# Performance work log

Hardware: AMD Instinct MI355X
Metric: run time of the kernel (lower is better)

The kernel has to match this reference:

```python
import jax, jax.numpy as jnp
import numpy as np

N, E, D_IN, D_H = 20000, 320000, 512, 512
ALPHA = 0.1
LAMBDA = 1.0

def setup_inputs() -> dict:
    key = jax.random.key(0)
    ks = jax.random.split(key, 12)
    feat = jax.random.normal(ks[0], (N, D_IN), dtype=jnp.float32)
    src = jax.random.randint(ks[1], (E,), 0, N, dtype=jnp.int32)
    dst = jax.random.randint(ks[2], (E,), 0, N, dtype=jnp.int32)
    s = 0.05
    fc_w = jax.random.normal(ks[3], (D_H, D_IN), dtype=jnp.float32) * s  # torch Linear: [out,in]
    fc_b = jax.random.normal(ks[4], (D_H,), dtype=jnp.float32) * s
    w1_1 = jax.random.normal(ks[5], (D_H, D_H), dtype=jnp.float32) * s
    w2_1 = jax.random.normal(ks[6], (D_H, D_H), dtype=jnp.float32) * s
    b_1 = jax.random.normal(ks[7], (D_H,), dtype=jnp.float32) * s
    w1_2 = jax.random.normal(ks[8], (D_H, D_H), dtype=jnp.float32) * s
    w2_2 = jax.random.normal(ks[9], (D_H, D_H), dtype=jnp.float32) * s
    b_2 = jax.random.normal(ks[10], (D_H,), dtype=jnp.float32) * s
    return {"feat": feat, "src": src, "dst": dst, "fc_w": fc_w, "fc_b": fc_b,
            "w1_1": w1_1, "w2_1": w2_1, "b_1": b_1,
            "w1_2": w1_2, "w2_2": w2_2, "b_2": b_2}


def _gcn2_layer(h, h0, src, dst, norm, w1, w2, b, layer):
    # DGL GCN2Conv (project_initial_features=False)
    beta = float(np.log(LAMBDA / layer + 1.0))
    x = h * norm                      # [N, D]
    agg = jax.ops.segment_sum(x[src], dst, num_segments=h.shape[0])  # SpMM: sum over in-neighbors
    agg = agg * norm
    f = agg * (1.0 - ALPHA)
    f0 = h0 * ALPHA
    rst = ((1.0 - beta) * f + beta * (f @ w1)
           + (1.0 - beta) * f0 + beta * (f0 @ w2) + b)
    return jax.nn.relu(rst)


def reference(feat, src, dst, fc_w, fc_b, w1_1, w2_1, b_1, w1_2, w2_2, b_2):
    n = feat.shape[0]
    h = feat @ fc_w.T + fc_b          # initial projection
    # symmetric norm from in-degrees (clamped at 1), as in DGL
    deg = jax.ops.segment_sum(jnp.ones_like(dst, dtype=h.dtype), dst, num_segments=n)
    norm = jnp.clip(deg, 1.0, None) ** -0.5
    norm = norm[:, None]
    res = _gcn2_layer(h, h, src, dst, norm, w1_1, w2_1, b_1, layer=1)
    out = _gcn2_layer(res, h, src, dst, norm, w1_2, w2_2, b_2, layer=2)
    return out
```

## Files before the change

kernel.cpp:

```cpp
#include <hip/hip_runtime.h>
#include <hip/hip_bf16.h>
#include <stdint.h>
#include <stddef.h>

typedef __bf16 bf16_t;
typedef __bf16 bf16x4 __attribute__((ext_vector_type(4)));
typedef __bf16 bf16x8 __attribute__((ext_vector_type(8)));
typedef float floatx4 __attribute__((ext_vector_type(4)));

#define NN 20000
#define EE 320000
#define DD 512
#define CAP 96
#define BETA1 0.6931471805599453f
#define BETA2 0.40546510810816444f

__device__ __forceinline__ void gload16(const bf16_t* g, bf16_t* l) {
  __builtin_amdgcn_global_load_lds((const __attribute__((address_space(1))) uint32_t*)g,
                                   (__attribute__((address_space(3))) uint32_t*)l, 16, 0, 0);
}

__global__ __launch_bounds__(256) void bucket_kernel(
    const int* __restrict__ src, const int* __restrict__ dst,
    int* __restrict__ cnt, int* __restrict__ esrc, int E) {
  int e = blockIdx.x * 256 + threadIdx.x;
  if (e < E) {
    int d = dst[e];
    int pos = atomicAdd(&cnt[d], 1);
    if (pos < CAP) esrc[d * CAP + pos] = src[e];
  }
}

#define PREP_BLOCKS 8106
__global__ __launch_bounds__(256) void prep_kernel(
    const float* __restrict__ feat, const float* __restrict__ fc_w,
    const float* __restrict__ w1_1, const float* __restrict__ w2_1,
    const float* __restrict__ w1_2, const float* __restrict__ w2_2,
    bf16_t* __restrict__ featb, bf16_t* __restrict__ bw0,
    bf16_t* __restrict__ bt1, bf16_t* __restrict__ bt2,
    int* __restrict__ cnt, int* __restrict__ esrc) {
  __shared__ bf16_t tile[32][33];
  int b = blockIdx.x, t = threadIdx.x;
  if (b < 5128) {
    const float* in = (b < 5000) ? feat : fc_w;
    bf16_t* out = (b < 5000) ? featb : bw0;
    size_t c = (size_t)(b < 5000 ? b : b - 5000) * 256 + t;
    const float* s = in + c * 8;
    float4 v0 = *(const float4*)s, v1 = *(const float4*)(s + 4);
    bf16x8 o = {(bf16_t)v0.x, (bf16_t)v0.y, (bf16_t)v0.z, (bf16_t)v0.w,
                (bf16_t)v1.x, (bf16_t)v1.y, (bf16_t)v1.z, (bf16_t)v1.w};
    *(bf16x8*)(out + c * 8) = o;
  } else if (b < 6152) {
    int base = (b < 5640) ? 5128 : 5640;
    const float* Wa = (b < 5640) ? w1_1 : w1_2;
    const float* Wb = (b < 5640) ? w2_1 : w2_2;
    bf16_t* bt = (b < 5640) ? bt1 : bt2;
    int bb = b - base;
    int n0 = (bb & 15) * 32;
    int k0 = (bb >> 4) * 32;
    int tx = t & 31, ty = t >> 5;
    const float* W = (k0 < 512) ? Wa : Wb;
    float sc = (k0 < 512) ? 1.0f : 0.1f;
    int kk = k0 & 511;
#pragma unroll
    for (int i = 0; i < 32; i += 8)
      tile[ty + i][tx] = (bf16_t)(sc * W[(size_t)(kk + ty + i) * 512 + n0 + tx]);
    __syncthreads();
#pragma unroll
    for (int i = 0; i < 32; i += 8)
      bt[(size_t)(n0 + ty + i) * 1024 + k0 + tx] = tile[tx][ty + i];
  } else if (b < 6231) {
    int i = (b - 6152) * 256 + t;
    if (i < NN) cnt[i] = 0;
  } else {
    int i = (b - 6231) * 256 + t;
    ((int4*)esrc)[i] = make_int4(0, 0, 0, 0);
  }
}

__global__ __launch_bounds__(256) void aggregate_kernel(
    const bf16_t* __restrict__ hs, const int* __restrict__ cnt,
    const int* __restrict__ esrc, bf16_t* __restrict__ Acat) {
  __shared__ bf16_t ring[4][3][4][512];
  const int w = threadIdx.x >> 6;
  const int lane = threadIdx.x & 63;
  const int node = blockIdx.x * 4 + w;
  const int* eb = esrc + (size_t)node * CAP;
  int ncnt = cnt[node];
  int n_e = ncnt < CAP ? ncnt : CAP;
  float nd = 0.9f * rsqrtf(fmaxf((float)ncnt, 1.0f));
  int nchunks = (n_e + 3) >> 2;

  float acc[8] = {};
  bf16_t* rb0 = &ring[w][0][0][lane * 8];
  bf16_t* rb1 = &ring[w][1][0][lane * 8];
  bf16_t* rb2 = &ring[w][2][0][lane * 8];

  asm volatile("s_waitcnt vmcnt(0)" ::: "memory");
  __builtin_amdgcn_sched_barrier(0);
  int4 i0 = *(const int4*)(eb);
  asm volatile("s_waitcnt vmcnt(0)" ::: "memory");
  __builtin_amdgcn_sched_barrier(0);
  int4 i1 = *(const int4*)(eb + 4);
  asm volatile("s_waitcnt vmcnt(0)" ::: "memory");
  __builtin_amdgcn_sched_barrier(0);
  gload16(hs + (size_t)i0.x * DD + lane * 8, rb0);
  gload16(hs + (size_t)i0.y * DD + lane * 8, rb0 + 512);
  gload16(hs + (size_t)i0.z * DD + lane * 8, rb0 + 1024);
  gload16(hs + (size_t)i0.w * DD + lane * 8, rb0 + 1536);
  int4 inext = *(const int4*)(eb + 8);
  gload16(hs + (size_t)i1.x * DD + lane * 8, rb1);
  gload16(hs + (size_t)i1.y * DD + lane * 8, rb1 + 512);
  gload16(hs + (size_t)i1.z * DD + lane * 8, rb1 + 1024);
  gload16(hs + (size_t)i1.w * DD + lane * 8, rb1 + 1536);

  for (int c = 0; c < nchunks; ++c) {
    asm volatile("s_waitcnt vmcnt(4)" ::: "memory");
    __builtin_amdgcn_sched_barrier(0);
    int4 iuse = inext;
    int off = (c + 3) * 4; off = off > CAP - 4 ? CAP - 4 : off;
    inext = *(const int4*)(eb + off);
    bf16_t* rbn = (c % 3 == 0) ? rb2 : (c % 3 == 1) ? rb0 : rb1;
    gload16(hs + (size_t)iuse.x * DD + lane * 8, rbn);
    gload16(hs + (size_t)iuse.y * DD + lane * 8, rbn + 512);
    gload16(hs + (size_t)iuse.z * DD + lane * 8, rbn + 1024);
    gload16(hs + (size_t)iuse.w * DD + lane * 8, rbn + 1536);
    bf16_t* rb = (c % 3 == 0) ? rb0 : (c % 3 == 1) ? rb1 : rb2;
    bf16x8 v0 = *(const bf16x8*)(rb);
    bf16x8 v1 = *(const bf16x8*)(rb + 512);
    bf16x8 v2 = *(const bf16x8*)(rb + 1024);
    bf16x8 v3 = *(const bf16x8*)(rb + 1536);
    int e0 = c * 4;
    if (e0 < n_e) {
#pragma unroll
      for (int k = 0; k < 8; ++k) acc[k] += (float)v0[k];
    }
    if (e0 + 1 < n_e) {
#pragma unroll
      for (int k = 0; k < 8; ++k) acc[k] += (float)v1[k];
    }
    if (e0 + 2 < n_e) {
#pragma unroll
      for (int k = 0; k < 8; ++k) acc[k] += (float)v2[k];
    }
    if (e0 + 3 < n_e) {
#pragma unroll
      for (int k = 0; k < 8; ++k) acc[k] += (float)v3[k];
    }
  }

  bf16x8 ob;
#pragma unroll
  for (int k = 0; k < 8; ++k) ob[k] = (bf16_t)(nd * acc[k]);
  *(bf16x8*)(Acat + (size_t)node * 1024 + lane * 8) = ob;
}

template <int MODE>
__global__ __launch_bounds__(256) void gemm_kernel(
    const bf16_t* __restrict__ A, const bf16_t* __restrict__ BT,
    int lda, int ldb, int K, int M,
    const float* __restrict__ bias,
    const bf16_t* __restrict__ acat_ro, float beta,
    float* __restrict__ outf, bf16_t* __restrict__ outb,
    bf16_t* __restrict__ acat2,
    const int* __restrict__ cnt) {
  __shared__ bf16_t As[2][64 * 64];
  __shared__ bf16_t Bs[2][128 * 64];

  const int bid = blockIdx.x;
  const int mt = (bid >> 5) * 8 + (bid & 7);
  const int nt = (bid >> 3) & 3;
  const int m0 = mt * 64;
  if (m0 >= M) return;
  const int n0 = nt * 128;

  const int t = threadIdx.x;
  const int lane = t & 63;
  const int w = t >> 6;
  const int wm = w & 1, wn = w >> 1;
  const int quad = lane >> 4, m16 = lane & 15;

  const int tr = t >> 3;
  const int gc = (t & 7) ^ (tr & 7);
  int arow0 = m0 + tr;      arow0 = arow0 < M ? arow0 : M - 1;
  int arow1 = m0 + tr + 32; arow1 = arow1 < M ? arow1 : M - 1;
  const bf16_t* agp0 = A + (size_t)arow0 * lda + gc * 8;
  const bf16_t* agp1 = A + (size_t)arow1 * lda + gc * 8;
  const bf16_t* bgp0 = BT + (size_t)(n0 + tr) * ldb + gc * 8;
  const bf16_t* bgp1 = BT + (size_t)(n0 + tr + 32) * ldb + gc * 8;
  const bf16_t* bgp2 = BT + (size_t)(n0 + tr + 64) * ldb + gc * 8;
  const bf16_t* bgp3 = BT + (size_t)(n0 + tr + 96) * ldb + gc * 8;

#define STAGE(buf, ko)                              \
  gload16(agp0 + (ko), &As[buf][t * 8]);            \
  gload16(agp1 + (ko), &As[buf][(t + 256) * 8]);    \
  gload16(bgp0 + (ko), &Bs[buf][t * 8]);            \
  gload16(bgp1 + (ko), &Bs[buf][(t + 256) * 8]);    \
  gload16(bgp2 + (ko), &Bs[buf][(t + 512) * 8]);    \
  gload16(bgp3 + (ko), &Bs[buf][(t + 768) * 8]);

  floatx4 acc[2][4] = {};
  const int niter = K >> 6;

  STAGE(0, 0)

  for (int kt = 0; kt < niter; ++kt) {
    __syncthreads();
    const int b = kt & 1;
    if (kt + 1 < niter) {
      const int ko = (kt + 1) * 64;
      STAGE(b ^ 1, ko)
    }

#pragma unroll
    for (int ks = 0; ks < 2; ++ks) {
      bf16x8 af[2], bfr[4];
#pragma unroll
      for (int i = 0; i < 2; ++i) {
        int arow = wm * 32 + i * 16 + m16;
        int cc = (ks * 4 + quad) ^ (arow & 7);
        af[i] = *(const bf16x8*)(&As[b][(arow * 8 + cc) * 8]);
      }
#pragma unroll
      for (int j = 0; j < 4; ++j) {
        int brow = wn * 64 + j * 16 + m16;
        int cc = (ks * 4 + quad) ^ (brow & 7);
        bfr[j] = *(const bf16x8*)(&Bs[b][(brow * 8 + cc) * 8]);
      }
#pragma unroll
      for (int i = 0; i < 2; ++i)
#pragma unroll
        for (int j = 0; j < 4; ++j)
          acc[i][j] = __builtin_amdgcn_mfma_f32_16x16x32_bf16(af[i], bfr[j], acc[i][j], 0, 0, 0);
    }
  }
#undef STAGE

  float rsv[2][4];
  if constexpr (MODE != 2) {
#pragma unroll
    for (int i = 0; i < 2; ++i)
#pragma unroll
      for (int p = 0; p < 4; ++p) {
        int row = m0 + wm * 32 + i * 16 + quad * 4 + p;
        int rowc = row < M ? row : M - 1;
        rsv[i][p] = rsqrtf(fmaxf((float)cnt[rowc], 1.0f));
      }
  }

#pragma unroll
  for (int i = 0; i < 2; ++i) {
#pragma unroll
    for (int j = 0; j < 4; ++j) {
      int col = n0 + wn * 64 + j * 16 + m16;
      float bv = bias[col];
#pragma unroll
      for (int p = 0; p < 4; ++p) {
        int row = m0 + wm * 32 + i * 16 + quad * 4 + p;
        if (row < M) {
          float v = acc[i][j][p];
          if constexpr (MODE == 0) {
            float hv = v + bv;
            acat2[(size_t)row * 1024 + 512 + col] = (bf16_t)hv;
            outb[(size_t)row * DD + col] = (bf16_t)(rsv[i][p] * hv);
          } else {
            size_t idx = (size_t)row * DD + col;
            float fsv = (float)acat_ro[(size_t)row * 1024 + col] +
                        0.1f * (float)acat_ro[(size_t)row * 1024 + 512 + col];
            float r = (1.0f - beta) * fsv + beta * v + bv;
            r = fmaxf(r, 0.0f);
            if constexpr (MODE == 1) outb[idx] = (bf16_t)(rsv[i][p] * r);
            else outf[idx] = r;
          }
        }
      }
    }
  }
}

extern "C" void kernel_launch(void* const* d_in, const int* in_sizes, int n_in,
                              void* d_out, int out_size, void* d_ws, size_t ws_size,
                              hipStream_t stream) {
  const float* feat = (const float*)d_in[0];
  const int* src = (const int*)d_in[1];
  const int* dst = (const int*)d_in[2];
  const float* fc_w = (const float*)d_in[3];
  const float* fc_b = (const float*)d_in[4];
  const float* w1_1 = (const float*)d_in[5];
  const float* w2_1 = (const float*)d_in[6];
  const float* b_1  = (const float*)d_in[7];
  const float* w1_2 = (const float*)d_in[8];
  const float* w2_2 = (const float*)d_in[9];
  const float* b_2  = (const float*)d_in[10];
  float* out = (float*)d_out;

  char* ws = (char*)d_ws;
  size_t off = 0;
  auto alloc = [&](size_t bytes) {
    char* p = ws + off;
    off += (bytes + 255) & ~(size_t)255;
    return p;
  };
  const size_t NDf = (size_t)NN * DD;
  bf16_t* res_bf = (bf16_t*)alloc(NDf * sizeof(bf16_t));
  bf16_t* featb  = (bf16_t*)alloc(NDf * sizeof(bf16_t));
  bf16_t* hs     = (bf16_t*)alloc(NDf * sizeof(bf16_t));
  bf16_t* Acat   = (bf16_t*)alloc((size_t)NN * 1024 * sizeof(bf16_t));
  bf16_t* BW0    = (bf16_t*)alloc((size_t)512 * 512 * sizeof(bf16_t));
  bf16_t* BT1    = (bf16_t*)alloc((size_t)512 * 1024 * sizeof(bf16_t));
  bf16_t* BT2    = (bf16_t*)alloc((size_t)512 * 1024 * sizeof(bf16_t));
  int*    cnt    = (int*)alloc((size_t)NN * sizeof(int));
  int*    esrc   = (int*)alloc(((size_t)NN * CAP + 64) * sizeof(int));

  prep_kernel<<<PREP_BLOCKS, 256, 0, stream>>>(feat, fc_w, w1_1, w2_1, w1_2, w2_2,
                                               featb, BW0, BT1, BT2, cnt, esrc);
  bucket_kernel<<<(EE + 255) / 256, 256, 0, stream>>>(src, dst, cnt, esrc, EE);

  gemm_kernel<0><<<1280, 256, 0, stream>>>(featb, BW0, 512, 512, 512, NN, fc_b,
                                           nullptr, 0.0f, nullptr, hs, Acat, cnt);

  aggregate_kernel<<<NN / 4, 256, 0, stream>>>(hs, cnt, esrc, Acat);
  gemm_kernel<1><<<1280, 256, 0, stream>>>(Acat, BT1, 1024, 1024, 1024, NN, b_1,
                                           Acat, BETA1, nullptr, res_bf, nullptr, cnt);

  aggregate_kernel<<<NN / 4, 256, 0, stream>>>(res_bf, cnt, esrc, Acat);
  gemm_kernel<2><<<1280, 256, 0, stream>>>(Acat, BT2, 1024, 1024, 1024, NN, b_2,
                                           Acat, BETA2, out, nullptr, nullptr, nullptr);
}
```

Measured before the change: 349.7 us.

## Switch aggregate gather ring from triple to double buffering

Shrinks the per-wave LDS ring in the neighbor-aggregation kernel from three 4-row stages to two, and restructures the prefetch so only one chunk of gathered rows is in flight ahead of consumption. An explicit vmcnt wait is added before reading the current buffer. This cuts LDS per block from 48KB to 32KB, which can allow more resident blocks per CU to hide gather latency. The cost is shallower software prefetch per wave.

```diff
diff --git a/kernel.cpp b/kernel.cpp
--- a/kernel.cpp
+++ b/kernel.cpp
@@ -81,7 +81,7 @@
 __global__ __launch_bounds__(256) void aggregate_kernel(
     const bf16_t* __restrict__ hs, const int* __restrict__ cnt,
     const int* __restrict__ esrc, bf16_t* __restrict__ Acat) {
-  __shared__ bf16_t ring[4][3][4][512];
+  __shared__ bf16_t ring[4][2][4][512];
   const int w = threadIdx.x >> 6;
   const int lane = threadIdx.x & 63;
   const int node = blockIdx.x * 4 + w;
@@ -92,40 +92,36 @@
   int nchunks = (n_e + 3) >> 2;
 
   float acc[8] = {};
-  bf16_t* rb0 = &ring[w][0][0][lane * 8];
-  bf16_t* rb1 = &ring[w][1][0][lane * 8];
-  bf16_t* rb2 = &ring[w][2][0][lane * 8];
+  bf16_t* r0base = &ring[w][0][0][lane * 8];
+  bf16_t* r1base = &ring[w][1][0][lane * 8];
+
+  int4 icur, inext;
 
   asm volatile("s_waitcnt vmcnt(0)" ::: "memory");
   __builtin_amdgcn_sched_barrier(0);
-  int4 i0 = *(const int4*)(eb);
+  icur = *(const int4*)(eb);
   asm volatile("s_waitcnt vmcnt(0)" ::: "memory");
   __builtin_amdgcn_sched_barrier(0);
-  int4 i1 = *(const int4*)(eb + 4);
-  asm volatile("s_waitcnt vmcnt(0)" ::: "memory");
-  __builtin_amdgcn_sched_barrier(0);
-  gload16(hs + (size_t)i0.x * DD + lane * 8, rb0);
-  gload16(hs + (size_t)i0.y * DD + lane * 8, rb0 + 512);
-  gload16(hs + (size_t)i0.z * DD + lane * 8, rb0 + 1024);
-  gload16(hs + (size_t)i0.w * DD + lane * 8, rb0 + 1536);
-  int4 inext = *(const int4*)(eb + 8);
-  gload16(hs + (size_t)i1.x * DD + lane * 8, rb1);
-  gload16(hs + (size_t)i1.y * DD + lane * 8, rb1 + 512);
-  gload16(hs + (size_t)i1.z * DD + lane * 8, rb1 + 1024);
-  gload16(hs + (size_t)i1.w * DD + lane * 8, rb1 + 1536);
+  inext = *(const int4*)(eb + 4);
+  gload16(hs + (size_t)icur.x * DD + lane * 8, r0base);
+  gload16(hs + (size_t)icur.y * DD + lane * 8, r0base + 512);
+  gload16(hs + (size_t)icur.z * DD + lane * 8, r0base + 1024);
+  gload16(hs + (size_t)icur.w * DD + lane * 8, r0base + 1536);
 
   for (int c = 0; c < nchunks; ++c) {
     asm volatile("s_waitcnt vmcnt(4)" ::: "memory");
     __builtin_amdgcn_sched_barrier(0);
     int4 iuse = inext;
-    int off = (c + 3) * 4; off = off > CAP - 4 ? CAP - 4 : off;
-    inext = *(const int4*)(eb + off);
-    bf16_t* rbn = (c % 3 == 0) ? rb2 : (c % 3 == 1) ? rb0 : rb1;
+    int off2 = (c + 2) * 4; off2 = off2 > CAP - 4 ? CAP - 4 : off2;
+    inext = *(const int4*)(eb + off2);
+    bf16_t* rbn = ((c + 1) & 1) ? r1base : r0base;
     gload16(hs + (size_t)iuse.x * DD + lane * 8, rbn);
     gload16(hs + (size_t)iuse.y * DD + lane * 8, rbn + 512);
     gload16(hs + (size_t)iuse.z * DD + lane * 8, rbn + 1024);
     gload16(hs + (size_t)iuse.w * DD + lane * 8, rbn + 1536);
-    bf16_t* rb = (c % 3 == 0) ? rb0 : (c % 3 == 1) ? rb1 : rb2;
+    asm volatile("s_waitcnt vmcnt(5)" ::: "memory");
+    __builtin_amdgcn_sched_barrier(0);
+    bf16_t* rb = (c & 1) ? r1base : r0base;
     bf16x8 v0 = *(const bf16x8*)(rb);
     bf16x8 v1 = *(const bf16x8*)(rb + 512);
     bf16x8 v2 = *(const bf16x8*)(rb + 1024);
```

Result: faster. 336.0 us (-3.9%).
